# Optimization experiments

Hardware: AMD Instinct MI355X
Metric: run time of the kernel (lower is better)

## Reference

```python
import jax, jax.numpy as jnp
import numpy as np

N_NODES = 6890
N_ANGLES = 8
K_CHEB = 15
N_DESC = 544
HIDDEN = 64
N_CLASS = 6890
M = N_ANGLES * N_NODES  # 55120, size of anisotropic Laplacian
DEG = 16
NNZ = M * DEG
BN_EPS = 1e-5


def setup_inputs() -> dict:
    key = jax.random.key(0)
    ks = jax.random.split(key, 16)
    x = jax.random.normal(ks[0], (N_NODES, N_DESC), dtype=jnp.float32)
    # sparse anisotropic Laplacian (M x M), ~DEG nnz per row
    rows = jnp.repeat(jnp.arange(M, dtype=jnp.int32), DEG)
    cols = jax.random.randint(ks[1], (NNZ,), 0, M, dtype=jnp.int32)
    vals = jax.random.normal(ks[2], (NNZ,), dtype=jnp.float32) * 0.1
    # conv1: (K, n_angles*n_desc, 64); conv2..6 stacked: (5, K, n_angles*64, 64)
    def xavier(k, shape, fan_in, fan_out):
        lim = np.sqrt(6.0 / (fan_in + fan_out))
        return jax.random.uniform(k, shape, jnp.float32, -lim, lim)
    W1 = xavier(ks[3], (K_CHEB, N_ANGLES * N_DESC, HIDDEN), N_ANGLES * N_DESC, HIDDEN)
    Wc = xavier(ks[4], (5, K_CHEB, N_ANGLES * HIDDEN, HIDDEN), N_ANGLES * HIDDEN, HIDDEN)
    conv_b = jnp.zeros((6, HIDDEN), jnp.float32)
    bn_gamma = jnp.ones((6, HIDDEN), jnp.float32)
    bn_beta = jnp.zeros((6, HIDDEN), jnp.float32)
    fc2_w = xavier(ks[5], (HIDDEN, 256), HIDDEN, 256)
    fc2_b = jnp.zeros((256,), jnp.float32)
    fc3_w = xavier(ks[6], (256, N_CLASS), 256, N_CLASS)
    fc3_b = jnp.zeros((N_CLASS,), jnp.float32)
    return {"x": x, "rows": rows, "cols": cols, "vals": vals,
            "W1": W1, "Wc": Wc, "conv_b": conv_b,
            "bn_gamma": bn_gamma, "bn_beta": bn_beta,
            "fc2_w": fc2_w, "fc2_b": fc2_b, "fc3_w": fc3_w, "fc3_b": fc3_b}


def _spmm(rows, cols, vals, T):
    # (M x M sparse) @ (M x C) via gather + segment-sum
    return jax.ops.segment_sum(vals[:, None] * T[cols], rows, num_segments=M)


def _acs_conv(x, rows, cols, vals, W, b):
    # x: (N, C). Chebyshev recurrence on the (A*N, C) angle-stacked signal.
    N, C = x.shape
    A = N_ANGLES

    def proj(T, Wk):
        # (A*N, C) -> (N, A*C) @ (A*C, out)
        return T.reshape(A, N, C).transpose(1, 0, 2).reshape(N, A * C) @ Wk

    T0 = jnp.tile(x, (A, 1))
    out = proj(T0, W[0])
    T1 = _spmm(rows, cols, vals, T0)
    out = out + proj(T1, W[1])
    for k in range(2, K_CHEB):
        T2 = 2.0 * _spmm(rows, cols, vals, T1) - T0
        out = out + proj(T2, W[k])
        T0, T1 = T1, T2
    return out + b


def _bn_relu(x, gamma, beta):
    # BatchNorm1d (training-mode batch stats, biased variance) + ReLU
    mean = jnp.mean(x, axis=0)
    var = jnp.var(x, axis=0)
    return jax.nn.relu((x - mean) * jax.lax.rsqrt(var + BN_EPS) * gamma + beta)


def reference(x, rows, cols, vals, W1, Wc, conv_b, bn_gamma, bn_beta,
              fc2_w, fc2_b, fc3_w, fc3_b):
    h = _bn_relu(_acs_conv(x, rows, cols, vals, W1, conv_b[0]), bn_gamma[0], bn_beta[0])
    for i in range(5):
        h = _bn_relu(_acs_conv(h, rows, cols, vals, Wc[i], conv_b[i + 1]),
                     bn_gamma[i + 1], bn_beta[i + 1])
    h = jax.nn.relu(h @ fc2_w + fc2_b)
    # dropout is identity at inference
    return h @ fc3_w + fc3_b
```

## Files before the change

### kernel.cpp

```cpp
#include <hip/hip_runtime.h>
#include <cstdint>
#include <cstddef>

#define NN 6890
#define NA 8
#define KC 15
#define ND 544
#define MR (NA * NN)
#define DEG 16
#define NNZ (MR * DEG)
#define BN_EPS 1e-5f
#define NRG 108
#define PB (NA * NRG)
#define NB256 6890
#define NB32  862
#define NB64  1723

typedef unsigned int u32;
typedef _Float16 f16;
typedef __attribute__((ext_vector_type(8))) _Float16 f16x8;
typedef __attribute__((ext_vector_type(4))) _Float16 f16x4;
typedef __attribute__((ext_vector_type(4))) float f32x4;

union U4H8 { uint4 q; f16 h[8]; f16x8 v; };

struct Slabs4 { const uint4* s[4]; };

__device__ __forceinline__ u32 packh(float a, float b) {
    union { f16 h[2]; u32 u; } c;
    c.h[0] = (f16)a; c.h[1] = (f16)b; return c.u;
}
__device__ __forceinline__ uint4 pack8h(const float* t) {
    uint4 m;
    m.x = packh(t[0], t[1]); m.y = packh(t[2], t[3]);
    m.z = packh(t[4], t[5]); m.w = packh(t[6], t[7]);
    return m;
}
__device__ __forceinline__ void acc8h(float* s, float v, uint4 g) {
    U4H8 c; c.q = g;
    #pragma unroll
    for (int i = 0; i < 8; ++i) s[i] += v * (float)c.h[i];
}

__global__ __launch_bounds__(256)
void prep_cv_kernel(const int* __restrict__ cols, const float* __restrict__ vals,
                    uint4* __restrict__ cvq)
{
    const int q = blockIdx.x * 256 + threadIdx.x;
    if (q >= NNZ / 4) return;
    const int4   c = ((const int4*)cols)[q];
    const float4 v = ((const float4*)vals)[q];
    uint4 o;
    o.x = ((u32)c.x & 0xffffu) | ((u32)c.y << 16);
    o.y = ((u32)c.z & 0xffffu) | ((u32)c.w << 16);
    o.z = packh(v.x, v.y);
    o.w = packh(v.z, v.w);
    cvq[q] = o;
}

template<int CC, bool BN>
__device__ __forceinline__
void tile_body(int bid, const float* __restrict__ X, int C_in, int c0,
               uint4* __restrict__ slab0, const float* __restrict__ bnp)
{
    constexpr int LPR = CC / 8;
    constexpr int RPB = 256 / LPR;
    const int tid = threadIdx.x;
    const int j = tid % LPR, rloc = tid / LPR;
    const int r = bid * RPB + rloc;
    if (r >= MR) return;
    const int n = r % NN;
    const float* xp = X + (size_t)n * C_in + c0 + 8 * j;
    const float4 t0 = *(const float4*)xp;
    const float4 t1 = *(const float4*)(xp + 4);
    float t[8] = { t0.x, t0.y, t0.z, t0.w, t1.x, t1.y, t1.z, t1.w };
    if (BN) {
        const int ch = c0 + 8 * j;
        #pragma unroll
        for (int i = 0; i < 8; ++i) {
            const float v = t[i] * bnp[ch + i] + bnp[64 + ch + i];
            t[i] = v > 0.f ? v : 0.f;
        }
    }
    slab0[(size_t)r * LPR + j] = pack8h(t);
}

__global__ __launch_bounds__(256)
void tile_l0_kernel(const float* __restrict__ X,
                    uint4* __restrict__ sA, uint4* __restrict__ sB,
                    uint4* __restrict__ sT)
{
    const int bid = blockIdx.x;
    if (bid < NB256)            tile_body<256, false>(bid, X, ND, 0, sA, nullptr);
    else if (bid < 2 * NB256)   tile_body<256, false>(bid - NB256, X, ND, 256, sB, nullptr);
    else                        tile_body<32,  false>(bid - 2 * NB256, X, ND, 512, sT, nullptr);
}

__global__ __launch_bounds__(256)
void tile64_bn_kernel(const float* __restrict__ X, uint4* __restrict__ slab0,
                      const float* __restrict__ bnp)
{
    tile_body<64, true>(blockIdx.x, X, 64, 0, slab0, bnp);
}

template<int CC, bool CHEB>
__device__ __forceinline__
void spmm_body(int bid, const uint4* __restrict__ sp, const uint4* __restrict__ sc,
               uint4* __restrict__ sw, const uint4* __restrict__ cvq, uint4* cvl)
{
    constexpr int LPR = CC / 8;
    constexpr int RPB = 256 / LPR;
    const int tid = threadIdx.x;
    const int j = tid % LPR, rloc = tid / LPR;
    const int r0 = bid * RPB;
    const int nrow = (MR - r0) < RPB ? (MR - r0) : RPB;
    for (int e = tid; e < nrow * 4; e += 256)
        cvl[e] = cvq[(size_t)r0 * 4 + e];
    __syncthreads();
    const int r = r0 + rloc;
    if (r >= MR) return;

    int c[16]; float v[16];
    #pragma unroll
    for (int q = 0; q < 4; ++q) {
        const uint4 cq = cvl[rloc * 4 + q];
        c[4 * q + 0] = cq.x & 0xffffu; c[4 * q + 1] = cq.x >> 16;
        c[4 * q + 2] = cq.y & 0xffffu; c[4 * q + 3] = cq.y >> 16;
        union { u32 u; f16 h[2]; } z, w_;
        z.u = cq.z; w_.u = cq.w;
        v[4 * q + 0] = (float)z.h[0]; v[4 * q + 1] = (float)z.h[1];
        v[4 * q + 2] = (float)w_.h[0]; v[4 * q + 3] = (float)w_.h[1];
    }
    float s[8] = {0.f, 0.f, 0.f, 0.f, 0.f, 0.f, 0.f, 0.f};
    #pragma unroll
    for (int d = 0; d < DEG; ++d)
        acc8h(s, v[d], sp[(size_t)c[d] * LPR + j]);
    float t[8];
    if (CHEB) {
        U4H8 p; p.q = sc[(size_t)r * LPR + j];
        #pragma unroll
        for (int i = 0; i < 8; ++i) t[i] = 2.f * s[i] - (float)p.h[i];
    } else {
        #pragma unroll
        for (int i = 0; i < 8; ++i) t[i] = s[i];
    }
    sw[(size_t)r * LPR + j] = pack8h(t);
}

template<bool FIRSTP>
__device__ __forceinline__
void proj_ld(f32x4 (&acc)[4], const float* __restrict__ part, int a, int rows0,
             int l, int w)
{
    const int hi16 = l >> 4;
    #pragma unroll
    for (int nt = 0; nt < 4; ++nt)
        #pragma unroll
        for (int rr = 0; rr < 4; ++rr) {
            const int orow = rows0 + w * 16 + hi16 * 4 + rr;
            float vv = 0.f;
            if (!FIRSTP && orow < NN)
                vv = part[((size_t)a * NN + orow) * 64 + nt * 16 + (l & 15)];
            acc[nt][rr] = vv;
        }
}

__device__ __forceinline__
void proj_st(const f32x4 (&acc)[4], float* __restrict__ part, int a, int rows0,
             int l, int w)
{
    const int hi16 = l >> 4;
    #pragma unroll
    for (int nt = 0; nt < 4; ++nt)
        #pragma unroll
        for (int rr = 0; rr < 4; ++rr) {
            const int orow = rows0 + w * 16 + hi16 * 4 + rr;
            if (orow < NN)
                part[((size_t)a * NN + orow) * 64 + nt * 16 + (l & 15)] = acc[nt][rr];
        }
}

template<int SCC, int NPROJ>
__device__ __forceinline__
void proj_accum(int a, int rows0, int l, int w, Slabs4 sl,
                const float* __restrict__ W, int C_in, int c0, int kbase,
                u32* WH, u32* WL, f32x4 (&acc)[4], bool presync)
{
    constexpr int LPRF   = SCC / 8;
    constexpr int SLICES = SCC >= 64 ? SCC / 64 : 1;
    constexpr int SCH    = SCC >= 64 ? 64 : SCC;
    constexpr int CCH    = SCH / 32;
    const int tid = threadIdx.x;
    const int hi16 = l >> 4;
    const int arow = rows0 + w * 16 + (l & 15);
    const int arc  = arow < NN ? arow : NN - 1;
    const size_t abase = (size_t)(a * NN + arc) * LPRF;

    #pragma unroll
    for (int p = 0; p < NPROJ; ++p) {
        const uint4* slab = sl.s[p];
        #pragma unroll
        for (int s = 0; s < SLICES; ++s) {
            const float* Wk = W + ((size_t)(kbase + p) * NA * C_in
                                   + (size_t)a * C_in + c0 + s * 64) * 64;
            if (p | s) __syncthreads();
            else if (presync) __syncthreads();
            for (int e = tid; e < CCH * 1024; e += 256) {
                const int i2 = e & 3;
                const int ll = (e >> 2) & 63;
                const int nt = (e >> 8) & 3;
                const int h  = e >> 10;
                const int cc  = h * 32 + (ll >> 4) * 8 + 2 * i2;
                const int col = nt * 16 + (ll & 15);
                const float w0 = Wk[(size_t)cc * 64 + col];
                const float w1 = Wk[(size_t)(cc + 1) * 64 + col];
                const f16 h0 = (f16)w0, h1 = (f16)w1;
                union { f16 h[2]; u32 u; } ph, pl;
                ph.h[0] = h0; ph.h[1] = h1;
                pl.h[0] = (f16)(w0 - (float)h0); pl.h[1] = (f16)(w1 - (float)h1);
                WH[e] = ph.u; WL[e] = pl.u;
            }
            __syncthreads();
            #pragma unroll
            for (int h = 0; h < CCH; ++h) {
                U4H8 af; af.q = slab[abase + s * 8 + h * 4 + hi16];
                #pragma unroll
                for (int nt = 0; nt < 4; ++nt) {
                    const int be = ((h * 4 + nt) * 64 + l) * 4;
                    U4H8 bh, bl;
                    bh.q = *(const uint4*)&WH[be];
                    bl.q = *(const uint4*)&WL[be];
                    acc[nt] = __builtin_amdgcn_mfma_f32_16x16x32_f16(af.v, bh.v, acc[nt], 0, 0, 0);
                    acc[nt] = __builtin_amdgcn_mfma_f32_16x16x32_f16(af.v, bl.v, acc[nt], 0, 0, 0);
                }
            }
        }
    }
}

template<bool CHEB>
__global__ __launch_bounds__(256)
void spmm_l0_kernel(const uint4* __restrict__ sAp, const uint4* __restrict__ sAc, uint4* __restrict__ sAw,
                    const uint4* __restrict__ sBp, const uint4* __restrict__ sBc, uint4* __restrict__ sBw,
                    const uint4* __restrict__ sTp, const uint4* __restrict__ sTc, uint4* __restrict__ sTw,
                    const uint4* __restrict__ cvq)
{
    __shared__ uint4 cvl[256];
    const int bid = blockIdx.x;
    if (bid < NB256)          spmm_body<256, CHEB>(bid, sAp, sAc, sAw, cvq, cvl);
    else if (bid < 2 * NB256) spmm_body<256, CHEB>(bid - NB256, sBp, sBc, sBw, cvq, cvl);
    else                      spmm_body<32,  CHEB>(bid - 2 * NB256, sTp, sTc, sTw, cvq, cvl);
}

template<bool FIRSTP>
__global__ __launch_bounds__(256)
void step_l0_proj_kernel(const uint4* __restrict__ sAp, const uint4* __restrict__ sAc, uint4* __restrict__ sAw,
                         const uint4* __restrict__ sBp, const uint4* __restrict__ sBc, uint4* __restrict__ sBw,
                         const uint4* __restrict__ sTp, const uint4* __restrict__ sTc, uint4* __restrict__ sTw,
                         const uint4* __restrict__ cvq, const float* __restrict__ W,
                         float* __restrict__ part, int kbase)
{
    __shared__ uint4 cvl[256];
    __shared__ u32 WH[2048];
    __shared__ u32 WL[2048];
    const int bid = blockIdx.x;
    if (bid < NB256)          { spmm_body<256, true>(bid, sAp, sAc, sAw, cvq, cvl); return; }
    if (bid < 2 * NB256)      { spmm_body<256, true>(bid - NB256, sBp, sBc, sBw, cvq, cvl); return; }
    if (bid < 2 * NB256 + NB32) { spmm_body<32, true>(bid - 2 * NB256, sTp, sTc, sTw, cvq, cvl); return; }
    const int pb = bid - (2 * NB256 + NB32);
    const int l = threadIdx.x & 63, w = threadIdx.x >> 6;
    const int a = pb / NRG, rows0 = (pb % NRG) * 64;
    f32x4 acc[4];
    proj_ld<FIRSTP>(acc, part, a, rows0, l, w);
    Slabs4 sa; sa.s[0] = sAc; sa.s[1] = sAp;
    Slabs4 sb; sb.s[0] = sBc; sb.s[1] = sBp;
    Slabs4 st; st.s[0] = sTc; st.s[1] = sTp;
    proj_accum<256, 2>(a, rows0, l, w, sa, W, ND, 0,   kbase, WH, WL, acc, false);
    proj_accum<256, 2>(a, rows0, l, w, sb, W, ND, 256, kbase, WH, WL, acc, true);
    proj_accum<32,  2>(a, rows0, l, w, st, W, ND, 512, kbase, WH, WL, acc, true);
    proj_st(acc, part, a, rows0, l, w);
}

__global__ __launch_bounds__(256)
void proj_l0_final_kernel(const uint4* __restrict__ sA, const uint4* __restrict__ sB,
                          const uint4* __restrict__ sT, const float* __restrict__ W,
                          float* __restrict__ part, int kbase)
{
    __shared__ u32 WH[2048];
    __shared__ u32 WL[2048];
    const int pb = blockIdx.x;
    const int l = threadIdx.x & 63, w = threadIdx.x >> 6;
    const int a = pb / NRG, rows0 = (pb % NRG) * 64;
    f32x4 acc[4];
    proj_ld<false>(acc, part, a, rows0, l, w);
    Slabs4 sa; sa.s[0] = sA;
    Slabs4 sb; sb.s[0] = sB;
    Slabs4 st; st.s[0] = sT;
    proj_accum<256, 1>(a, rows0, l, w, sa, W, ND, 0,   kbase, WH, WL, acc, false);
    proj_accum<256, 1>(a, rows0, l, w, sb, W, ND, 256, kbase, WH, WL, acc, true);
    proj_accum<32,  1>(a, rows0, l, w, st, W, ND, 512, kbase, WH, WL, acc, true);
    proj_st(acc, part, a, rows0, l, w);
}

template<bool CHEB>
__global__ __launch_bounds__(256)
void spmm64_kernel(const uint4* __restrict__ sp, const uint4* __restrict__ sc,
                   uint4* __restrict__ sw, const uint4* __restrict__ cvq)
{
    __shared__ uint4 cvl[128];
    spmm_body<64, CHEB>(blockIdx.x, sp, sc, sw, cvq, cvl);
}

template<bool FIRSTP>
__global__ __launch_bounds__(256)
void step64_proj4_kernel(const uint4* __restrict__ sp, const uint4* __restrict__ sc,
                         uint4* __restrict__ sw, Slabs4 prj,
                         const uint4* __restrict__ cvq, const float* __restrict__ W,
                         float* __restrict__ part, int kbase)
{
    __shared__ uint4 cvl[128];
    __shared__ u32 WH[2048];
    __shared__ u32 WL[2048];
    const int bid = blockIdx.x;
    if (bid < NB64) { spmm_body<64, true>(bid, sp, sc, sw, cvq, cvl); return; }
    const int pb = bid - NB64;
    const int l = threadIdx.x & 63, w = threadIdx.x >> 6;
    const int a = pb / NRG, rows0 = (pb % NRG) * 64;
    f32x4 acc[4];
    proj_ld<FIRSTP>(acc, part, a, rows0, l, w);
    proj_accum<64, 4>(a, rows0, l, w, prj, W, 64, 0, kbase, WH, WL, acc, false);
    proj_st(acc, part, a, rows0, l, w);
}

__global__ __launch_bounds__(256)
void proj64_final_kernel(Slabs4 prj, const float* __restrict__ W,
                         float* __restrict__ part, int kbase)
{
    __shared__ u32 WH[2048];
    __shared__ u32 WL[2048];
    const int pb = blockIdx.x;
    const int l = threadIdx.x & 63, w = threadIdx.x >> 6;
    const int a = pb / NRG, rows0 = (pb % NRG) * 64;
    f32x4 acc[4];
    proj_ld<false>(acc, part, a, rows0, l, w);
    proj_accum<64, 3>(a, rows0, l, w, prj, W, 64, 0, kbase, WH, WL, acc, false);
    proj_st(acc, part, a, rows0, l, w);
}

__global__ void bn_reduce_kernel(const float* __restrict__ part, float* __restrict__ acc)
{
    const int e = blockIdx.x * blockDim.x + threadIdx.x;
    if (e >= NN * 64) return;
    float s = 0.f;
    #pragma unroll
    for (int a = 0; a < NA; ++a) s += part[(size_t)a * NN * 64 + e];
    acc[e] = s;
}

__global__ __launch_bounds__(256)
void bn_stats_kernel(const float* __restrict__ acc, const float* __restrict__ gamma,
                     const float* __restrict__ beta, float* __restrict__ bnp)
{
    const int h = blockIdx.x;
    float s = 0.f, sq = 0.f;
    for (int n = threadIdx.x; n < NN; n += 256) {
        const float v = acc[(size_t)n * 64 + h];
        s += v; sq += v * v;
    }
    __shared__ float ls[256], lq[256];
    ls[threadIdx.x] = s; lq[threadIdx.x] = sq;
    __syncthreads();
    for (int st = 128; st > 0; st >>= 1) {
        if (threadIdx.x < st) { ls[threadIdx.x] += ls[threadIdx.x + st]; lq[threadIdx.x] += lq[threadIdx.x + st]; }
        __syncthreads();
    }
    if (threadIdx.x == 0) {
        const float mean = ls[0] / (float)NN;
        const float var  = lq[0] / (float)NN - mean * mean;
        const float sc   = gamma[h] / sqrtf(var + BN_EPS);
        bnp[h]      = sc;
        bnp[64 + h] = beta[h] - mean * sc;
    }
}

__global__ void bn_apply_kernel(const float* __restrict__ acc, const float* __restrict__ bnp,
                                float* __restrict__ H)
{
    const int e = blockIdx.x * blockDim.x + threadIdx.x;
    if (e >= NN * 64) return;
    const int h = e & 63;
    const float v = acc[e] * bnp[h] + bnp[64 + h];
    H[e] = v > 0.f ? v : 0.f;
}

__global__ __launch_bounds__(256)
void fc2_kernel(const float* __restrict__ A, const float* __restrict__ B,
                const float* __restrict__ bias,
                f16* __restrict__ Oh, f16* __restrict__ Ol)
{
    constexpr int Kk = 64, Nn = 256;
    __shared__ float As[16][132];
    __shared__ float Bs[16][132];
    const int tx = threadIdx.x & 15, ty = threadIdx.x >> 4;
    const int m0 = blockIdx.y * 128, n0 = blockIdx.x * 128;
    const bool full = (m0 + 128 <= NN);
    float acc[8][8] = {};
    for (int k0 = 0; k0 < Kk; k0 += 16) {
        if (full) {
            #pragma unroll
            for (int e = threadIdx.x; e < 512; e += 256) {
                const int i = e >> 2, q = e & 3;
                const float4 a4 = *(const float4*)&A[(size_t)(m0 + i) * Kk + k0 + 4 * q];
                As[4 * q + 0][i] = a4.x; As[4 * q + 1][i] = a4.y;
                As[4 * q + 2][i] = a4.z; As[4 * q + 3][i] = a4.w;
            }
        } else {
            for (int e = threadIdx.x; e < 128 * 16; e += 256) {
                const int i = e >> 4, kk = e & 15;
                const int row = m0 + i;
                As[kk][i] = (row < NN) ? A[(size_t)row * Kk + k0 + kk] : 0.f;
            }
        }
        #pragma unroll
        for (int e = threadIdx.x; e < 512; e += 256) {
            const int kk = e >> 5, q = e & 31;
            *(float4*)&Bs[kk][4 * q] = *(const float4*)&B[(size_t)(k0 + kk) * Nn + n0 + 4 * q];
        }
        __syncthreads();
        #pragma unroll
        for (int kk = 0; kk < 16; ++kk) {
            float av[8], bv[8];
            *(float4*)&av[0] = *(const float4*)&As[kk][ty * 4];
            *(float4*)&av[4] = *(const float4*)&As[kk][64 + ty * 4];
            *(float4*)&bv[0] = *(const float4*)&Bs[kk][tx * 4];
            *(float4*)&bv[4] = *(const float4*)&Bs[kk][64 + tx * 4];
            #pragma unroll
            for (int i = 0; i < 8; ++i)
                #pragma unroll
                for (int jj = 0; jj < 8; ++jj)
                    acc[i][jj] += av[i] * bv[jj];
        }
        __syncthreads();
    }
    #pragma unroll
    for (int i = 0; i < 8; ++i) {
        const int row = m0 + (i < 4 ? ty * 4 + i : 64 + ty * 4 + (i - 4));
        if (row >= NN) continue;
        #pragma unroll
        for (int g = 0; g < 2; ++g) {
            const int colg = n0 + (g ? 64 : 0) + tx * 4;
            f16x4 vh, vl;
            #pragma unroll
            for (int jj = 0; jj < 4; ++jj) {
                float v = acc[i][g * 4 + jj] + bias[colg + jj];
                v = fmaxf(v, 0.f);
                const f16 h = (f16)v;
                vh[jj] = h; vl[jj] = (f16)(v - (float)h);
            }
            const size_t ob = ((size_t)(colg >> 3) * NN + row) * 8 + (colg & 7);
            *(f16x4*)&Oh[ob] = vh;
            *(f16x4*)&Ol[ob] = vl;
        }
    }
}

__global__ __launch_bounds__(256)
void w3_split_kernel(const float* __restrict__ W, f16* __restrict__ Wh, f16* __restrict__ Wl)
{
    __shared__ float t[64][65];
    const int tid = threadIdx.x;
    const int n0 = blockIdx.x * 64, k0 = blockIdx.y * 64;
    for (int e = tid; e < 64 * 64; e += 256) {
        const int kk = e >> 6, nn = e & 63;
        const int gn = n0 + nn;
        t[kk][nn] = (gn < NN) ? W[(size_t)(k0 + kk) * NN + gn] : 0.f;
    }
    __syncthreads();
    for (int e = tid; e < 64 * 8; e += 256) {
        const int nn = e >> 3, c8 = e & 7;
        const int gn = n0 + nn;
        if (gn >= NN) continue;
        const size_t ob = ((size_t)((k0 >> 3) + c8) * NN + gn) * 8;
        f16 vh[8], vl[8];
        #pragma unroll
        for (int i = 0; i < 8; ++i) {
            const float w = t[c8 * 8 + i][nn];
            const f16 h = (f16)w;
            vh[i] = h; vl[i] = (f16)(w - (float)h);
        }
        *(uint4*)&Wh[ob] = *(const uint4*)vh;
        *(uint4*)&Wl[ob] = *(const uint4*)vl;
    }
}

__global__ __launch_bounds__(256)
void fc3_mfma_kernel(const f16* __restrict__ Ah, const f16* __restrict__ Al,
                     const f16* __restrict__ Bh, const f16* __restrict__ Bl,
                     const float* __restrict__ bias, float* __restrict__ C)
{
    const int o = blockIdx.x;
    const int xcd = o & 7, jj0 = o >> 3;
    const int wg = (xcd < 4 ? xcd * 365 : 4 * 365 + (xcd - 4) * 364) + jj0;
    const int band = wg / 486, inb = wg % 486;
    const int mt = inb / 9, nt = band * 9 + inb % 9;
    const int m0 = mt * 128, n0 = nt * 128;

    const int tid = threadIdx.x, l = tid & 63, w = tid >> 6;
    const int wm = w >> 1, wn = w & 1, hi16 = l >> 4;

    size_t aoff[4], boff[4];
    #pragma unroll
    for (int mf = 0; mf < 4; ++mf) {
        int row = m0 + wm * 64 + mf * 16 + (l & 15);
        if (row > NN - 1) row = NN - 1;
        aoff[mf] = (size_t)row * 8;
    }
    #pragma unroll
    for (int nf = 0; nf < 4; ++nf) {
        int col = n0 + wn * 64 + nf * 16 + (l & 15);
        if (col > NN - 1) col = NN - 1;
        boff[nf] = (size_t)col * 8;
    }

    f32x4 acc[4][4];
    #pragma unroll
    for (int mf = 0; mf < 4; ++mf)
        #pragma unroll
        for (int nf = 0; nf < 4; ++nf)
            acc[mf][nf] = (f32x4){0.f, 0.f, 0.f, 0.f};

    for (int k0 = 0; k0 < 256; k0 += 32) {
        const size_t cb = (size_t)((k0 >> 3) + hi16) * NN * 8;
        f16x8 ah[4], al[4], bh[4], bl[4];
        #pragma unroll
        for (int mf = 0; mf < 4; ++mf) {
            ah[mf] = *(const f16x8*)(Ah + cb + aoff[mf]);
            al[mf] = *(const f16x8*)(Al + cb + aoff[mf]);
        }
        #pragma unroll
        for (int nf = 0; nf < 4; ++nf) {
            bh[nf] = *(const f16x8*)(Bh + cb + boff[nf]);
            bl[nf] = *(const f16x8*)(Bl + cb + boff[nf]);
        }
        #pragma unroll
        for (int mf = 0; mf < 4; ++mf)
            #pragma unroll
            for (int nf = 0; nf < 4; ++nf) {
                acc[mf][nf] = __builtin_amdgcn_mfma_f32_16x16x32_f16(ah[mf], bh[nf], acc[mf][nf], 0, 0, 0);
                acc[mf][nf] = __builtin_amdgcn_mfma_f32_16x16x32_f16(ah[mf], bl[nf], acc[mf][nf], 0, 0, 0);
                acc[mf][nf] = __builtin_amdgcn_mfma_f32_16x16x32_f16(al[mf], bh[nf], acc[mf][nf], 0, 0, 0);
            }
    }

    #pragma unroll
    for (int mf = 0; mf < 4; ++mf) {
        #pragma unroll
        for (int nf = 0; nf < 4; ++nf) {
            const int col = n0 + wn * 64 + nf * 16 + (l & 15);
            if (col >= NN) continue;
            const float bv = bias[col];
            #pragma unroll
            for (int rr = 0; rr < 4; ++rr) {
                const int row = m0 + wm * 64 + mf * 16 + hi16 * 4 + rr;
                if (row < NN)
                    C[(size_t)row * NN + col] = acc[mf][nf][rr] + bv;
            }
        }
    }
}

extern "C" void kernel_launch(void* const* d_in, const int* in_sizes, int n_in,
                              void* d_out, int out_size, void* d_ws, size_t ws_size,
                              hipStream_t stream)
{
    (void)in_sizes; (void)n_in; (void)out_size; (void)ws_size;
    const float* x     = (const float*)d_in[0];
    const int*   cols  = (const int*)  d_in[2];
    const float* vals  = (const float*)d_in[3];
    const float* W1    = (const float*)d_in[4];
    const float* Wc    = (const float*)d_in[5];
    const float* gamma = (const float*)d_in[7];
    const float* beta  = (const float*)d_in[8];
    const float* fc2w  = (const float*)d_in[9];
    const float* fc2b  = (const float*)d_in[10];
    const float* fc3w  = (const float*)d_in[11];
    const float* fc3b  = (const float*)d_in[12];

    const size_t MT = (size_t)MR * 64;

    const size_t SL256 = (size_t)MR * 32;
    const size_t SL32  = (size_t)MR * 4;
    uint4* ringA = (uint4*)d_out;
    uint4* ringB = ringA + 3 * SL256;
    uint4* ringT = ringB + 3 * SL256;
    auto slA = [&](int k) { return ringA + (size_t)(k % 3) * SL256; };
    auto slB = [&](int k) { return ringB + (size_t)(k % 3) * SL256; };
    auto slT = [&](int k) { return ringT + (size_t)(k % 3) * SL32; };

    char* base = (char*)d_ws;
    size_t off = 0;
    uint4* cvq  = (uint4*)(base + off); off += (size_t)(NNZ / 4) * 16;
    uint4* ring5 = (uint4*)(base + off); off += 5 * (size_t)MR * 8 * 16;
    float* part = (float*)(base + off); off += MT * 4;
    float* acc  = (float*)(base + off); off += (size_t)NN * 64 * 4;
    float* H    = (float*)(base + off); off += (size_t)NN * 64 * 4;
    f16* f2h    = (f16*)(base + off);   off += (size_t)NN * 256 * 2;
    f16* f2l    = (f16*)(base + off);   off += (size_t)NN * 256 * 2;
    f16* W3h    = (f16*)(base + off);   off += (size_t)NN * 256 * 2;
    f16* W3l    = (f16*)(base + off);   off += (size_t)NN * 256 * 2;
    float* bnp  = (float*)(base + off);
    const size_t SL64 = (size_t)MR * 8;
    auto sl5 = [&](int k) { return ring5 + (size_t)(k % 5) * SL64; };

    prep_cv_kernel<<<(NNZ / 4 + 255) / 256, 256, 0, stream>>>(cols, vals, cvq);
    w3_split_kernel<<<dim3(108, 4), 256, 0, stream>>>(fc3w, W3h, W3l);

    {
        const float* W = W1;
        tile_l0_kernel<<<2 * NB256 + NB32, 256, 0, stream>>>(x, slA(0), slB(0), slT(0));
        spmm_l0_kernel<false><<<2 * NB256 + NB32, 256, 0, stream>>>(
            slA(0), slA(0), slA(1), slB(0), slB(0), slB(1), slT(0), slT(0), slT(1), cvq);
        for (int k = 2; k < KC; ++k) {
            if (k & 1) {
                spmm_l0_kernel<true><<<2 * NB256 + NB32, 256, 0, stream>>>(
                    slA(k - 1), slA(k - 2), slA(k), slB(k - 1), slB(k - 2), slB(k),
                    slT(k - 1), slT(k - 2), slT(k), cvq);
            } else if (k == 2) {
                step_l0_proj_kernel<true><<<2 * NB256 + NB32 + PB, 256, 0, stream>>>(
                    slA(k - 1), slA(k - 2), slA(k), slB(k - 1), slB(k - 2), slB(k),
                    slT(k - 1), slT(k - 2), slT(k), cvq, W, part, k - 2);
            } else {
                step_l0_proj_kernel<false><<<2 * NB256 + NB32 + PB, 256, 0, stream>>>(
                    slA(k - 1), slA(k - 2), slA(k), slB(k - 1), slB(k - 2), slB(k),
                    slT(k - 1), slT(k - 2), slT(k), cvq, W, part, k - 2);
            }
        }
        proj_l0_final_kernel<<<PB, 256, 0, stream>>>(slA(14), slB(14), slT(14), W, part, 14);
        bn_reduce_kernel<<<(NN * 64 + 255) / 256, 256, 0, stream>>>(part, acc);
        bn_stats_kernel<<<64, 256, 0, stream>>>(acc, gamma, beta, bnp);
    }

    for (int li = 1; li < 6; ++li) {
        const float* W = Wc + (size_t)(li - 1) * KC * (NA * 64) * 64;
        tile64_bn_kernel<<<NB64, 256, 0, stream>>>(acc, sl5(0), bnp);
        spmm64_kernel<false><<<NB64, 256, 0, stream>>>(sl5(0), sl5(0), sl5(1), cvq);
        for (int k = 2; k < KC; ++k) {
            if (k == 4 || k == 8 || k == 12) {
                Slabs4 prj;
                prj.s[0] = sl5(k - 4); prj.s[1] = sl5(k - 3);
                prj.s[2] = sl5(k - 2); prj.s[3] = sl5(k - 1);
                if (k == 4)
                    step64_proj4_kernel<true ><<<NB64 + PB, 256, 0, stream>>>(
                        sl5(k - 1), sl5(k - 2), sl5(k), prj, cvq, W, part, k - 4);
                else
                    step64_proj4_kernel<false><<<NB64 + PB, 256, 0, stream>>>(
                        sl5(k - 1), sl5(k - 2), sl5(k), prj, cvq, W, part, k - 4);
            } else {
                spmm64_kernel<true><<<NB64, 256, 0, stream>>>(sl5(k - 1), sl5(k - 2), sl5(k), cvq);
            }
        }
        Slabs4 prjf;
        prjf.s[0] = sl5(12); prjf.s[1] = sl5(13); prjf.s[2] = sl5(14); prjf.s[3] = sl5(14);
        proj64_final_kernel<<<PB, 256, 0, stream>>>(prjf, W, part, 12);
        bn_reduce_kernel<<<(NN * 64 + 255) / 256, 256, 0, stream>>>(part, acc);
        bn_stats_kernel<<<64, 256, 0, stream>>>(acc, gamma + li * 64, beta + li * 64, bnp);
    }

    bn_apply_kernel<<<(NN * 64 + 255) / 256, 256, 0, stream>>>(acc, bnp, H);
    fc2_kernel<<<dim3(2, 54), 256, 0, stream>>>(H, fc2w, fc2b, f2h, f2l);
    fc3_mfma_kernel<<<2916, 256, 0, stream>>>(f2h, f2l, W3h, W3l, fc3b, (float*)d_out);
}
```

Before: 3.876 ms.

## Split layer-0 Chebyshev recurrence into sequential per-channel-chunk phases

Instead of running the layer-0 recurrence on all 544 channels at once (three slabs per kernel), the channel dimension is processed in three independent passes (256, 256, 32 channels), each with its own full 15-step recurrence and projection accumulation into the shared partial output. Each pass reuses a single smaller 3-slot ring, so the live working set per step is roughly half as large and may fit better in the last-level cache during random gathers. The trade-off is about three times as many kernel launches for layer 0, and the gather index/value stream is re-read once per pass.

Result: slower. 4.034 ms (+4.1%).

```diff
diff --git a/kernel.cpp b/kernel.cpp
--- a/kernel.cpp
+++ b/kernel.cpp
@@ -12,8 +12,6 @@
 #define BN_EPS 1e-5f
 #define NRG 108
 #define PB (NA * NRG)
-#define NB256 6890
-#define NB32  862
 #define NB64  1723
 
 typedef unsigned int u32;
@@ -85,15 +83,12 @@
     slab0[(size_t)r * LPR + j] = pack8h(t);
 }
 
-__global__ __launch_bounds__(256)
-void tile_l0_kernel(const float* __restrict__ X,
-                    uint4* __restrict__ sA, uint4* __restrict__ sB,
-                    uint4* __restrict__ sT)
-{
-    const int bid = blockIdx.x;
-    if (bid < NB256)            tile_body<256, false>(bid, X, ND, 0, sA, nullptr);
-    else if (bid < 2 * NB256)   tile_body<256, false>(bid - NB256, X, ND, 256, sB, nullptr);
-    else                        tile_body<32,  false>(bid - 2 * NB256, X, ND, 512, sT, nullptr);
+template<int CC>
+__global__ __launch_bounds__(256)
+void tile_any_kernel(const float* __restrict__ X, int C_in, int c0,
+                     uint4* __restrict__ slab0)
+{
+    tile_body<CC, false>(blockIdx.x, X, C_in, c0, slab0, nullptr);
 }
 
 __global__ __launch_bounds__(256)
@@ -145,6 +140,15 @@
         for (int i = 0; i < 8; ++i) t[i] = s[i];
     }
     sw[(size_t)r * LPR + j] = pack8h(t);
+}
+
+template<int CC, bool CHEB>
+__global__ __launch_bounds__(256)
+void spmm_any_kernel(const uint4* __restrict__ sp, const uint4* __restrict__ sc,
+                     uint4* __restrict__ sw, const uint4* __restrict__ cvq)
+{
+    __shared__ uint4 cvl[256];
+    spmm_body<CC, CHEB>(blockIdx.x, sp, sc, sw, cvq, cvl);
 }
 
 template<bool FIRSTP>
@@ -238,53 +242,32 @@
     }
 }
 
-template<bool CHEB>
-__global__ __launch_bounds__(256)
-void spmm_l0_kernel(const uint4* __restrict__ sAp, const uint4* __restrict__ sAc, uint4* __restrict__ sAw,
-                    const uint4* __restrict__ sBp, const uint4* __restrict__ sBc, uint4* __restrict__ sBw,
-                    const uint4* __restrict__ sTp, const uint4* __restrict__ sTc, uint4* __restrict__ sTw,
-                    const uint4* __restrict__ cvq)
-{
-    __shared__ uint4 cvl[256];
-    const int bid = blockIdx.x;
-    if (bid < NB256)          spmm_body<256, CHEB>(bid, sAp, sAc, sAw, cvq, cvl);
-    else if (bid < 2 * NB256) spmm_body<256, CHEB>(bid - NB256, sBp, sBc, sBw, cvq, cvl);
-    else                      spmm_body<32,  CHEB>(bid - 2 * NB256, sTp, sTc, sTw, cvq, cvl);
-}
-
-template<bool FIRSTP>
-__global__ __launch_bounds__(256)
-void step_l0_proj_kernel(const uint4* __restrict__ sAp, const uint4* __restrict__ sAc, uint4* __restrict__ sAw,
-                         const uint4* __restrict__ sBp, const uint4* __restrict__ sBc, uint4* __restrict__ sBw,
-                         const uint4* __restrict__ sTp, const uint4* __restrict__ sTc, uint4* __restrict__ sTw,
-                         const uint4* __restrict__ cvq, const float* __restrict__ W,
-                         float* __restrict__ part, int kbase)
+template<int CC, bool FIRSTP>
+__global__ __launch_bounds__(256)
+void step_any_proj_kernel(const uint4* __restrict__ sp, const uint4* __restrict__ sc,
+                          uint4* __restrict__ sw, const uint4* __restrict__ cvq,
+                          const float* __restrict__ W, float* __restrict__ part,
+                          int C_in, int c0, int kbase, int NB)
 {
     __shared__ uint4 cvl[256];
     __shared__ u32 WH[2048];
     __shared__ u32 WL[2048];
     const int bid = blockIdx.x;
-    if (bid < NB256)          { spmm_body<256, true>(bid, sAp, sAc, sAw, cvq, cvl); return; }
-    if (bid < 2 * NB256)      { spmm_body<256, true>(bid - NB256, sBp, sBc, sBw, cvq, cvl); return; }
-    if (bid < 2 * NB256 + NB32) { spmm_body<32, true>(bid - 2 * NB256, sTp, sTc, sTw, cvq, cvl); return; }
-    const int pb = bid - (2 * NB256 + NB32);
+    if (bid < NB) { spmm_body<CC, true>(bid, sp, sc, sw, cvq, cvl); return; }
+    const int pb = bid - NB;
     const int l = threadIdx.x & 63, w = threadIdx.x >> 6;
     const int a = pb / NRG, rows0 = (pb % NRG) * 64;
     f32x4 acc[4];
     proj_ld<FIRSTP>(acc, part, a, rows0, l, w);
-    Slabs4 sa; sa.s[0] = sAc; sa.s[1] = sAp;
-    Slabs4 sb; sb.s[0] = sBc; sb.s[1] = sBp;
-    Slabs4 st; st.s[0] = sTc; st.s[1] = sTp;
-    proj_accum<256, 2>(a, rows0, l, w, sa, W, ND, 0,   kbase, WH, WL, acc, false);
-    proj_accum<256, 2>(a, rows0, l, w, sb, W, ND, 256, kbase, WH, WL, acc, true);
-    proj_accum<32,  2>(a, rows0, l, w, st, W, ND, 512, kbase, WH, WL, acc, true);
+    Slabs4 s2; s2.s[0] = sc; s2.s[1] = sp;
+    proj_accum<CC, 2>(a, rows0, l, w, s2, W, C_in, c0, kbase, WH, WL, acc, false);
     proj_st(acc, part, a, rows0, l, w);
 }
 
-__global__ __launch_bounds__(256)
-void proj_l0_final_kernel(const uint4* __restrict__ sA, const uint4* __restrict__ sB,
-                          const uint4* __restrict__ sT, const float* __restrict__ W,
-                          float* __restrict__ part, int kbase)
+template<int CC>
+__global__ __launch_bounds__(256)
+void proj_any_final_kernel(const uint4* __restrict__ sl, const float* __restrict__ W,
+                           float* __restrict__ part, int C_in, int c0, int kproj)
 {
     __shared__ u32 WH[2048];
     __shared__ u32 WL[2048];
@@ -293,22 +276,9 @@
     const int a = pb / NRG, rows0 = (pb % NRG) * 64;
     f32x4 acc[4];
     proj_ld<false>(acc, part, a, rows0, l, w);
-    Slabs4 sa; sa.s[0] = sA;
-    Slabs4 sb; sb.s[0] = sB;
-    Slabs4 st; st.s[0] = sT;
-    proj_accum<256, 1>(a, rows0, l, w, sa, W, ND, 0,   kbase, WH, WL, acc, false);
-    proj_accum<256, 1>(a, rows0, l, w, sb, W, ND, 256, kbase, WH, WL, acc, true);
-    proj_accum<32,  1>(a, rows0, l, w, st, W, ND, 512, kbase, WH, WL, acc, true);
+    Slabs4 s1; s1.s[0] = sl;
+    proj_accum<CC, 1>(a, rows0, l, w, s1, W, C_in, c0, kproj, WH, WL, acc, false);
     proj_st(acc, part, a, rows0, l, w);
-}
-
-template<bool CHEB>
-__global__ __launch_bounds__(256)
-void spmm64_kernel(const uint4* __restrict__ sp, const uint4* __restrict__ sc,
-                   uint4* __restrict__ sw, const uint4* __restrict__ cvq)
-{
-    __shared__ uint4 cvl[128];
-    spmm_body<64, CHEB>(blockIdx.x, sp, sc, sw, cvq, cvl);
 }
 
 template<bool FIRSTP>
@@ -318,7 +288,7 @@
                          const uint4* __restrict__ cvq, const float* __restrict__ W,
                          float* __restrict__ part, int kbase)
 {
-    __shared__ uint4 cvl[128];
+    __shared__ uint4 cvl[256];
     __shared__ u32 WH[2048];
     __shared__ u32 WL[2048];
     const int bid = blockIdx.x;
@@ -569,6 +539,31 @@
     }
 }
 
+template<int CC>
+static void run_phase(bool first, const float* X, int c0, const uint4* cvq,
+                      const float* W, uint4* ring, float* part, hipStream_t stream)
+{
+    constexpr int RPB = 256 / (CC / 8);
+    const int NB = (MR + RPB - 1) / RPB;
+    const size_t SLOT = (size_t)MR * (CC / 8);
+    auto sl = [&](int k) { return ring + (size_t)(k % 3) * SLOT; };
+
+    tile_any_kernel<CC><<<NB, 256, 0, stream>>>(X, ND, c0, sl(0));
+    spmm_any_kernel<CC, false><<<NB, 256, 0, stream>>>(sl(0), sl(0), sl(1), cvq);
+    for (int k = 2; k < KC; ++k) {
+        if (k & 1) {
+            spmm_any_kernel<CC, true><<<NB, 256, 0, stream>>>(sl(k - 1), sl(k - 2), sl(k), cvq);
+        } else if (first && k == 2) {
+            step_any_proj_kernel<CC, true ><<<NB + PB, 256, 0, stream>>>(
+                sl(k - 1), sl(k - 2), sl(k), cvq, W, part, ND, c0, k - 2, NB);
+        } else {
+            step_any_proj_kernel<CC, false><<<NB + PB, 256, 0, stream>>>(
+                sl(k - 1), sl(k - 2), sl(k), cvq, W, part, ND, c0, k - 2, NB);
+        }
+    }
+    proj_any_final_kernel<CC><<<PB, 256, 0, stream>>>(sl(KC - 1), W, part, ND, c0, KC - 1);
+}
+
 extern "C" void kernel_launch(void* const* d_in, const int* in_sizes, int n_in,
                               void* d_out, int out_size, void* d_ws, size_t ws_size,
                               hipStream_t stream)
@@ -588,14 +583,8 @@
 
     const size_t MT = (size_t)MR * 64;
 
-    const size_t SL256 = (size_t)MR * 32;
-    const size_t SL32  = (size_t)MR * 4;
-    uint4* ringA = (uint4*)d_out;
-    uint4* ringB = ringA + 3 * SL256;
-    uint4* ringT = ringB + 3 * SL256;
-    auto slA = [&](int k) { return ringA + (size_t)(k % 3) * SL256; };
-    auto slB = [&](int k) { return ringB + (size_t)(k % 3) * SL256; };
-    auto slT = [&](int k) { return ringT + (size_t)(k % 3) * SL32; };
+    uint4* ringAB = (uint4*)d_out;
+    uint4* ringT  = ringAB + 3 * (size_t)MR * 32;
 
     char* base = (char*)d_ws;
     size_t off = 0;
@@ -616,26 +605,9 @@
     w3_split_kernel<<<dim3(108, 4), 256, 0, stream>>>(fc3w, W3h, W3l);
 
     {
-        const float* W = W1;
-        tile_l0_kernel<<<2 * NB256 + NB32, 256, 0, stream>>>(x, slA(0), slB(0), slT(0));
-        spmm_l0_kernel<false><<<2 * NB256 + NB32, 256, 0, stream>>>(
-            slA(0), slA(0), slA(1), slB(0), slB(0), slB(1), slT(0), slT(0), slT(1), cvq);
-        for (int k = 2; k < KC; ++k) {
-            if (k & 1) {
-                spmm_l0_kernel<true><<<2 * NB256 + NB32, 256, 0, stream>>>(
-                    slA(k - 1), slA(k - 2), slA(k), slB(k - 1), slB(k - 2), slB(k),
-                    slT(k - 1), slT(k - 2), slT(k), cvq);
-            } else if (k == 2) {
-                step_l0_proj_kernel<true><<<2 * NB256 + NB32 + PB, 256, 0, stream>>>(
-                    slA(k - 1), slA(k - 2), slA(k), slB(k - 1), slB(k - 2), slB(k),
-                    slT(k - 1), slT(k - 2), slT(k), cvq, W, part, k - 2);
-            } else {
-                step_l0_proj_kernel<false><<<2 * NB256 + NB32 + PB, 256, 0, stream>>>(
-                    slA(k - 1), slA(k - 2), slA(k), slB(k - 1), slB(k - 2), slB(k),
-                    slT(k - 1), slT(k - 2), slT(k), cvq, W, part, k - 2);
-            }
-        }
-        proj_l0_final_kernel<<<PB, 256, 0, stream>>>(slA(14), slB(14), slT(14), W, part, 14);
+        run_phase<256>(true,  x, 0,   cvq, W1, ringAB, part, stream);
+        run_phase<256>(false, x, 256, cvq, W1, ringAB, part, stream);
+        run_phase<32 >(false, x, 512, cvq, W1, ringT,  part, stream);
         bn_reduce_kernel<<<(NN * 64 + 255) / 256, 256, 0, stream>>>(part, acc);
         bn_stats_kernel<<<64, 256, 0, stream>>>(acc, gamma, beta, bnp);
     }
@@ -643,7 +615,7 @@
     for (int li = 1; li < 6; ++li) {
         const float* W = Wc + (size_t)(li - 1) * KC * (NA * 64) * 64;
         tile64_bn_kernel<<<NB64, 256, 0, stream>>>(acc, sl5(0), bnp);
-        spmm64_kernel<false><<<NB64, 256, 0, stream>>>(sl5(0), sl5(0), sl5(1), cvq);
+        spmm_any_kernel<64, false><<<NB64, 256, 0, stream>>>(sl5(0), sl5(0), sl5(1), cvq);
         for (int k = 2; k < KC; ++k) {
             if (k == 4 || k == 8 || k == 12) {
                 Slabs4 prj;
@@ -656,7 +628,7 @@
                     step64_proj4_kernel<false><<<NB64 + PB, 256, 0, stream>>>(
                         sl5(k - 1), sl5(k - 2), sl5(k), prj, cvq, W, part, k - 4);
             } else {
-                spmm64_kernel<true><<<NB64, 256, 0, stream>>>(sl5(k - 1), sl5(k - 2), sl5(k), cvq);
+                spmm_any_kernel<64, true><<<NB64, 256, 0, stream>>>(sl5(k - 1), sl5(k - 2), sl5(k), cvq);
             }
         }
         Slabs4 prjf;
```
